# Kernel tuning notes

Measured on AMD Instinct MI355X. Metric: run time of the kernel, lower is better.

The kernel has to match this reference:

```python
import jax, jax.numpy as jnp
import numpy as np

# Scaled-up constants (GRID_SIZE=96)
AFFINE_HIDDEN_DIM = 128
ATTENTION_DIM = 256
EMBEDDING_DIM = 512
MAX_CONTRAST = 1.8
RANGE_SIZE = 4
NUM_RANGE_BLOCKS = 13824   # (96//4)**3
NUM_DOMAIN_BLOCKS = 1728   # (96//8)**3
SOFTMAX_TEMPERATURE = 0.25


def setup_inputs() -> dict:
    key = jax.random.key(0)
    ks = jax.random.split(key, 17)
    E, A, H = EMBEDDING_DIM, ATTENTION_DIM, AFFINE_HIDDEN_DIM
    NR, ND = NUM_RANGE_BLOCKS, NUM_DOMAIN_BLOCKS
    s_lin = 1.0 / np.sqrt(E)  # torch Linear default init scale
    return {
        "pooled_domains": jax.random.normal(ks[0], (ND, RANGE_SIZE, RANGE_SIZE, RANGE_SIZE), jnp.float32),
        "range_latents": jax.random.normal(ks[1], (NR, E), jnp.float32),
        "domain_latents": jax.random.normal(ks[2], (ND, E), jnp.float32),
        "range_positional": jax.random.normal(ks[3], (NR, E), jnp.float32),
        "domain_positional": jax.random.normal(ks[4], (ND, E), jnp.float32),
        "W_rproj": jax.random.normal(ks[5], (E, A), jnp.float32) * s_lin,
        "b_rproj": jax.random.normal(ks[6], (A,), jnp.float32) * s_lin,
        "W_dproj": jax.random.normal(ks[7], (E, A), jnp.float32) * s_lin,
        "b_dproj": jax.random.normal(ks[8], (A,), jnp.float32) * s_lin,
        "W_rcon": jax.random.normal(ks[9], (E, H), jnp.float32) * s_lin,
        "b_rcon": jax.random.normal(ks[10], (H,), jnp.float32) * s_lin,
        "W_dcon": jax.random.normal(ks[11], (E, H), jnp.float32) * s_lin,
        "b_dcon": jax.random.normal(ks[12], (H,), jnp.float32) * s_lin,
        "W_roff": jax.random.normal(ks[13], (E, H), jnp.float32) * s_lin,
        "b_roff": jax.random.normal(ks[14], (H,), jnp.float32) * s_lin,
        "W_doff": jax.random.normal(ks[15], (E, H), jnp.float32) * s_lin,
        "b_doff": jax.random.normal(ks[16], (H,), jnp.float32) * s_lin,
    }


def reference(pooled_domains, range_latents, domain_latents,
              range_positional, domain_positional,
              W_rproj, b_rproj, W_dproj, b_dproj,
              W_rcon, b_rcon, W_dcon, b_dcon,
              W_roff, b_roff, W_doff, b_doff):
    range_base = range_latents + range_positional      # [NR, E]
    domain_base = domain_latents + domain_positional   # [ND, E]

    range_repr = range_base @ W_rproj + b_rproj        # [NR, A]
    domain_repr = domain_base @ W_dproj + b_dproj      # [ND, A]

    inv_sqrt_h = 1.0 / np.sqrt(AFFINE_HIDDEN_DIM).astype(np.float32)
    range_con = range_base @ W_rcon + b_rcon           # [NR, H]
    domain_con = domain_base @ W_dcon + b_dcon         # [ND, H]
    contrast = jnp.tanh((range_con @ domain_con.T) * inv_sqrt_h) * MAX_CONTRAST  # [NR, ND]

    range_off = range_base @ W_roff + b_roff
    domain_off = domain_base @ W_doff + b_doff
    offset = jnp.tanh((range_off @ domain_off.T) * inv_sqrt_h)  # [NR, ND]

    scale = 1.0 / (np.sqrt(ATTENTION_DIM).astype(np.float32) * SOFTMAX_TEMPERATURE)
    logits = (range_repr @ domain_repr.T) * scale      # [NR, ND]
    weights = jax.nn.softmax(logits, axis=-1)          # [NR, ND]

    domain_flat = pooled_domains.reshape(NUM_DOMAIN_BLOCKS, -1)   # [ND, 64]
    scaled_domains = (weights * contrast) @ domain_flat           # [NR, 64]
    offset_effective = jnp.sum(weights * offset, axis=1, keepdims=True)  # [NR, 1]
    decoded = (scaled_domains + offset_effective).reshape(-1, RANGE_SIZE, RANGE_SIZE, RANGE_SIZE)
    return decoded
```

## Files before the change

kernel.cpp:

```cpp
#include <hip/hip_runtime.h>
#include <stdint.h>

#define NRB 13824
#define NDB 1728
#define EDIM 512
#define SPLIT 18
#define DPB (NDB/SPLIT)
#define TILES (DPB/32)

typedef __attribute__((ext_vector_type(8))) _Float16 h8;
typedef __attribute__((ext_vector_type(4))) _Float16 hh4;
typedef __attribute__((ext_vector_type(4))) float f4;
typedef __attribute__((ext_vector_type(4))) unsigned short us4;

typedef __attribute__((address_space(3))) void lds_void;
typedef const __attribute__((address_space(1))) void gbl_void;

#define MFMA(a,b,c) __builtin_amdgcn_mfma_f32_16x16x32_f16(a,b,c,0,0,0)

static __device__ __forceinline__ ushort f2h(float f){
  union { _Float16 h; ushort u; } cv;
  cv.h = (_Float16)f;
  return cv.u;
}

static __device__ __forceinline__ float tanh_fast(float x){
  float ax = __builtin_fabsf(x);
  float t = __builtin_amdgcn_exp2f(ax * -2.8853900817779268f);
  float r = (1.0f - t) * __builtin_amdgcn_rcpf(1.0f + t);
  return __builtin_copysignf(r, x);
}

__global__ void prep_kernel(
    const float* __restrict__ pooled,
    const float* __restrict__ rlat, const float* __restrict__ dlat,
    const float* __restrict__ rpos, const float* __restrict__ dpos,
    const float* __restrict__ Wrp, const float* __restrict__ brp,
    const float* __restrict__ Wdp, const float* __restrict__ bdp,
    const float* __restrict__ Wrc, const float* __restrict__ brc,
    const float* __restrict__ Wdc, const float* __restrict__ bdc,
    const float* __restrict__ Wro, const float* __restrict__ bro,
    const float* __restrict__ Wdo2, const float* __restrict__ bdo2,
    ushort* __restrict__ rb, ushort* __restrict__ db,
    ushort* __restrict__ Wr_t, ushort* __restrict__ Wd_t,
    float* __restrict__ br_c, float* __restrict__ bd_c,
    ushort* __restrict__ dflt)
{
  const int NRE = NRB*EDIM, NDE = NDB*EDIM;
  int i0 = blockIdx.x*blockDim.x + threadIdx.x;
  int stride = gridDim.x*blockDim.x;
  for (int i=i0; i<NRE; i+=stride) rb[i] = f2h(rlat[i]+rpos[i]);
  for (int i=i0; i<NDE; i+=stride) db[i] = f2h(dlat[i]+dpos[i]);
  for (int i=i0; i<512*512; i+=stride){
    int n = i>>9, k = i&511;
    float vr = (n<256) ? Wrp[k*256+n] : ((n<384) ? Wrc[k*128+(n-256)] : Wro[k*128+(n-384)]);
    float vd = (n<256) ? Wdp[k*256+n] : ((n<384) ? Wdc[k*128+(n-256)] : Wdo2[k*128+(n-384)]);
    Wr_t[i] = f2h(vr); Wd_t[i] = f2h(vd);
  }
  for (int i=i0; i<512; i+=stride){
    br_c[i] = (i<256) ? brp[i] : ((i<384) ? brc[i-256] : bro[i-384]);
    bd_c[i] = (i<256) ? bdp[i] : ((i<384) ? bdc[i-256] : bdo2[i-384]);
  }
  for (int i=i0; i<64*NDB; i+=stride){
    int c = i/NDB, d = i - c*NDB;
    dflt[i] = f2h(pooled[d*64+c]);
  }
}

__global__ __launch_bounds__(256) void gemm_feats(
    const ushort* __restrict__ Ar, const ushort* __restrict__ Btr,
    const float* __restrict__ biasr, ushort* __restrict__ Cr,
    const ushort* __restrict__ Ad, const ushort* __restrict__ Btd,
    const float* __restrict__ biasd, ushort* __restrict__ Cd)
{
  const ushort* A;  const ushort* Bt; const float* bias; ushort* C; int M; int bx;
  if ((int)blockIdx.x < 108){ A=Ar; Bt=Btr; bias=biasr; C=Cr; M=NRB; bx=blockIdx.x; }
  else                      { A=Ad; Bt=Btd; bias=biasd; C=Cd; M=NDB; bx=blockIdx.x-108; }

  __shared__ ushort As[128*32];
  __shared__ ushort Bs[128*32];
  const int tid = threadIdx.x;
  const int lane = tid & 63;
  const int wave = tid >> 6;
  const int l15 = lane & 15;
  const int lhi = lane >> 4;
  const int row0 = bx * 128;
  const int col0 = blockIdx.y * 128;
  const int wr = (wave>>1)*64;
  const int wc = (wave&1)*64;

  f4 acc[4][4] = {};
  char* Ab = (char*)As; char* Bb = (char*)Bs;

  for (int k0=0; k0<EDIM; k0+=32){
    __syncthreads();
    #pragma unroll
    for (int c=0;c<2;c++){
      int L = (tid + c*256)*16;
      int r = L>>6;
      int kb = L&63;
      int kbs = kb ^ ((r&3)<<4);
      int ra = row0 + r; if (ra > M-1) ra = M-1;
      const ushort* srcA = A + (size_t)ra*EDIM + k0 + (kbs>>1);
      const ushort* srcB = Bt + (size_t)(col0+r)*EDIM + k0 + (kbs>>1);
      __builtin_amdgcn_global_load_lds((gbl_void*)srcA, (lds_void*)(Ab + L), 16, 0, 0);
      __builtin_amdgcn_global_load_lds((gbl_void*)srcB, (lds_void*)(Bb + L), 16, 0, 0);
    }
    __syncthreads();
    h8 af[4], bf[4];
    #pragma unroll
    for (int i=0;i<4;i++){
      int rowa = wr + i*16 + l15;
      af[i] = *(const h8*)(Ab + (((rowa*64) + lhi*16) ^ ((rowa&3)<<4)));
      int rowb = wc + i*16 + l15;
      bf[i] = *(const h8*)(Bb + (((rowb*64) + lhi*16) ^ ((rowb&3)<<4)));
    }
    #pragma unroll
    for (int i=0;i<4;i++){
      #pragma unroll
      for (int j=0;j<4;j++){
        acc[i][j] = MFMA(af[i], bf[j], acc[i][j]);
      }
    }
  }

  #pragma unroll
  for (int j=0;j<4;j++){
    int col = col0 + wc + j*16 + l15;
    float bv = bias[col];
    #pragma unroll
    for (int i=0;i<4;i++){
      #pragma unroll
      for (int r=0;r<4;r++){
        int row = row0 + wr + i*16 + lhi*4 + r;
        if (row < M) C[(size_t)row*EDIM + col] = f2h(acc[i][j][r] + bv);
      }
    }
  }
}

__global__ __launch_bounds__(512, 2) void attn_kernel(
    const ushort* __restrict__ rfeat,
    const ushort* __restrict__ dfeat,
    const ushort* __restrict__ dflt,
    ushort* __restrict__ accbuf,
    float* __restrict__ mlbuf)
{
  __shared__ ushort DF[DPB*512];
  __shared__ ushort PT[8][16*32];

  const int tid  = threadIdx.x;
  const int wave = tid >> 6;
  const int lane = tid & 63;
  const int l15  = lane & 15;
  const int lhi  = lane >> 4;
  const int wrow = blockIdx.x*128 + wave*16;
  const int by   = blockIdx.y;
  const int dbase = by * DPB;

  constexpr float CL = 0.25f * 1.4426950408889634f;
  constexpr float CH = 0.08838834764831845f;

  char* DFb = (char*)DF;
  char* PTb = (char*)PT[wave];

  #pragma unroll
  for (int c=0;c<12;c++){
    int id = tid + c*512;
    int dom = id >> 6;
    h8 v = *(const h8*)(dfeat + (size_t)(dbase+dom)*EDIM + (id&63)*8);
    *(h8*)(DFb + ((id*16) ^ ((dom&7)<<4))) = v;
  }

  h8 q[16];
  {
    const ushort* qr = rfeat + (size_t)(wrow + l15)*EDIM + lhi*8;
    #pragma unroll
    for (int c=0;c<16;c++) q[c] = *(const h8*)(qr + c*32);
  }

  f4 acc[4] = {};
  float m = -1e30f, lsum = 0.f, offa = 0.f;
  const int sb = (lane & 48) + ((lane >> 4) << 2);

  __syncthreads();

  for (int t=0; t<TILES; ++t){
    const int d0 = dbase + t*32;
    const int dloc = t*32;

    f4 SL[2] = {}, SC[2] = {}, SO[2] = {};
    #pragma unroll
    for (int ct=0; ct<2; ++ct){
      const int dom = dloc + ct*16 + l15;
      const int swz = (dom&7)<<4;
      const int base = dom*1024 + lhi*16;
      #pragma unroll
      for (int c=0;c<8;c++){
        h8 b = *(const h8*)(DFb + ((base + c*64) ^ swz));
        SL[ct] = MFMA(b, q[c], SL[ct]);
      }
      #pragma unroll
      for (int c=8;c<12;c++){
        h8 b = *(const h8*)(DFb + ((base + c*64) ^ swz));
        SC[ct] = MFMA(b, q[c], SC[ct]);
      }
      #pragma unroll
      for (int c=12;c<16;c++){
        h8 b = *(const h8*)(DFb + ((base + c*64) ^ swz));
        SO[ct] = MFMA(b, q[c], SO[ct]);
      }
    }

    float lm = fmaxf(
        fmaxf(fmaxf(SL[0][0],SL[0][1]), fmaxf(SL[0][2],SL[0][3])),
        fmaxf(fmaxf(SL[1][0],SL[1][1]), fmaxf(SL[1][2],SL[1][3]))) * CL;
    lm = fmaxf(lm, __shfl_xor(lm, 16, 64));
    lm = fmaxf(lm, __shfl_xor(lm, 32, 64));
    float mn = fmaxf(m, lm);
    float al = __builtin_amdgcn_exp2f(m - mn);
    m = mn;
    lsum *= al; offa *= al;

    us4 w0, w1;
    #pragma unroll
    for (int r=0;r<4;r++){
      float p0 = __builtin_amdgcn_exp2f(SL[0][r]*CL - mn);
      float p1 = __builtin_amdgcn_exp2f(SL[1][r]*CL - mn);
      lsum += p0 + p1;
      float c0 = tanh_fast(SC[0][r]*CH)*1.8f;
      float c1 = tanh_fast(SC[1][r]*CH)*1.8f;
      float o0 = tanh_fast(SO[0][r]*CH);
      float o1 = tanh_fast(SO[1][r]*CH);
      offa += p0*o0 + p1*o1;
      w0[r] = f2h(p0*c0);
      w1[r] = f2h(p1*c1);
    }
    {
      const int wbase = l15*64;
      const int xs = (l15&3)<<4;
      *(us4*)(PTb + ((wbase + lhi*8) ^ xs))      = w0;
      *(us4*)(PTb + ((wbase + 32 + lhi*8) ^ xs)) = w1;
    }

    __builtin_amdgcn_sched_barrier(0);

    {
      float alr[4];
      #pragma unroll
      for (int r=0;r<4;r++) alr[r] = __shfl(al, sb + r, 64);
      #pragma unroll
      for (int nt=0; nt<4; nt++){
        acc[nt][0]*=alr[0]; acc[nt][1]*=alr[1];
        acc[nt][2]*=alr[2]; acc[nt][3]*=alr[3];
      }
      h8 pa = *(const h8*)(PTb + ((l15*64 + lhi*16) ^ ((l15&3)<<4)));
      #pragma unroll
      for (int nt=0; nt<4; nt++){
        int n = nt*16 + l15;
        h8 vb = *(const h8*)(dflt + (size_t)n*NDB + d0 + lhi*8);
        acc[nt] = MFMA(pa, vb, acc[nt]);
      }
    }

    __builtin_amdgcn_sched_barrier(0);
  }

  float ls = lsum, oa = offa;
  ls += __shfl_xor(ls, 16, 64); ls += __shfl_xor(ls, 32, 64);
  oa += __shfl_xor(oa, 16, 64); oa += __shfl_xor(oa, 32, 64);

  #pragma unroll
  for (int r=0;r<4;r++){
    int row = wrow + lhi*4 + r;
    size_t base = ((size_t)by*NRB + row)*64;
    #pragma unroll
    for (int nt=0; nt<4; nt++){
      accbuf[base + nt*16 + l15] = f2h(acc[nt][r]);
    }
  }
  if (lane < 16){
    size_t mo = ((size_t)by*NRB + wrow + l15)*4;
    mlbuf[mo+0] = m;
    mlbuf[mo+1] = ls;
    mlbuf[mo+2] = oa;
  }
}

#define CROWS 16
__global__ __launch_bounds__(256) void combine_kernel(
    const ushort* __restrict__ accbuf,
    const float* __restrict__ mlbuf,
    float* __restrict__ out)
{
  __shared__ float wS[CROWS][SPLIT+1];
  __shared__ float c0S[CROWS], iTS[CROWS];
  const int rb = blockIdx.x;
  const int tid = threadIdx.x;

  if (tid < CROWS){
    int row = rb*CROWS + tid;
    float M = -1e30f;
    float m[SPLIT], l[SPLIT], o[SPLIT];
    #pragma unroll
    for (int s=0;s<SPLIT;s++){
      size_t off = ((size_t)s*NRB + row)*4;
      m[s]=mlbuf[off]; l[s]=mlbuf[off+1]; o[s]=mlbuf[off+2];
      M = fmaxf(M, m[s]);
    }
    float T=0.f, C=0.f;
    #pragma unroll
    for (int s=0;s<SPLIT;s++){
      float w = __builtin_amdgcn_exp2f(m[s]-M);
      wS[tid][s]=w; T += l[s]*w; C += o[s]*w;
    }
    c0S[tid]=C; iTS[tid]=1.0f/T;
  }
  __syncthreads();

  const int row_l = tid>>4;
  const int cb = (tid&15)*4;
  const int row = rb*CROWS + row_l;
  float res[4] = {};
  #pragma unroll
  for (int s=0;s<SPLIT;s++){
    float w = wS[row_l][s];
    hh4 v = *(const hh4*)(accbuf + ((size_t)s*NRB + row)*64 + cb);
    #pragma unroll
    for (int j=0;j<4;j++) res[j] += (float)v[j]*w;
  }
  float C = c0S[row_l], iT = iTS[row_l];
  #pragma unroll
  for (int j=0;j<4;j++) out[(size_t)row*64 + cb + j] = (res[j]+C)*iT;
}

extern "C" void kernel_launch(void* const* d_in, const int* in_sizes, int n_in,
                              void* d_out, int out_size, void* d_ws, size_t ws_size,
                              hipStream_t stream) {
  const float* pooled = (const float*)d_in[0];
  const float* rlat   = (const float*)d_in[1];
  const float* dlat   = (const float*)d_in[2];
  const float* rpos   = (const float*)d_in[3];
  const float* dpos   = (const float*)d_in[4];
  const float* Wrp    = (const float*)d_in[5];
  const float* brp    = (const float*)d_in[6];
  const float* Wdp    = (const float*)d_in[7];
  const float* bdp    = (const float*)d_in[8];
  const float* Wrc    = (const float*)d_in[9];
  const float* brc    = (const float*)d_in[10];
  const float* Wdc    = (const float*)d_in[11];
  const float* bdc    = (const float*)d_in[12];
  const float* Wro    = (const float*)d_in[13];
  const float* bro    = (const float*)d_in[14];
  const float* Wdo2   = (const float*)d_in[15];
  const float* bdo2   = (const float*)d_in[16];

  char* ws = (char*)d_ws;
  size_t off = 0;
  ushort* rb    = (ushort*)(ws + off); off += (size_t)NRB*EDIM*2;
  ushort* db    = (ushort*)(ws + off); off += (size_t)NDB*EDIM*2;
  ushort* Wr_t  = (ushort*)(ws + off); off += (size_t)512*512*2;
  ushort* Wd_t  = (ushort*)(ws + off); off += (size_t)512*512*2;
  float*  br_c  = (float*)(ws + off);  off += 512*4;
  float*  bd_c  = (float*)(ws + off);  off += 512*4;
  ushort* rfeat = (ushort*)(ws + off); off += (size_t)NRB*EDIM*2;
  ushort* dfeat = (ushort*)(ws + off); off += (size_t)NDB*EDIM*2;
  ushort* dflt  = (ushort*)(ws + off); off += (size_t)64*NDB*2;
  ushort* accb  = (ushort*)(ws + off); off += (size_t)SPLIT*NRB*64*2;
  float*  mlb   = (float*)(ws + off);  off += (size_t)SPLIT*NRB*4*4;

  prep_kernel<<<2048, 256, 0, stream>>>(pooled, rlat, dlat, rpos, dpos,
      Wrp, brp, Wdp, bdp, Wrc, brc, Wdc, bdc, Wro, bro, Wdo2, bdo2,
      rb, db, Wr_t, Wd_t, br_c, bd_c, dflt);

  gemm_feats<<<dim3(122,4), 256, 0, stream>>>(rb, Wr_t, br_c, rfeat,
                                              db, Wd_t, bd_c, dfeat);

  attn_kernel<<<dim3(108, SPLIT), 512, 0, stream>>>(rfeat, dfeat, dflt, accb, mlb);
  combine_kernel<<<NRB/CROWS, 256, 0, stream>>>(accb, mlb, (float*)d_out);
}
```

Measured before the change: 132.9 us.

## Compute all score tiles first and use exact max instead of online softmax

Instead of an online softmax that rescales running sums and the output accumulators after every tile, all score tiles (logits, contrast, offset) are computed up front and kept in registers. A single global row max is taken before the exponentials, which removes the per-tile shuffles, exp of the correction factor and accumulator rescaling. The cost is much higher register pressure, since TILES=3 tiles times three score sets are live at once, which could cut occupancy or cause spills.

```diff
diff --git a/kernel.cpp b/kernel.cpp
--- a/kernel.cpp
+++ b/kernel.cpp
@@ -180,58 +180,65 @@
   }
 
   f4 acc[4] = {};
-  float m = -1e30f, lsum = 0.f, offa = 0.f;
   const int sb = (lane & 48) + ((lane >> 4) << 2);
+  (void)sb;
 
   __syncthreads();
 
+  f4 SL[TILES][2] = {}, SC[TILES][2] = {}, SO[TILES][2] = {};
+  #pragma unroll
+  for (int t=0; t<TILES; ++t){
+    #pragma unroll
+    for (int ct=0; ct<2; ++ct){
+      const int dom = t*32 + ct*16 + l15;
+      const int swz = (dom&7)<<4;
+      const int base = dom*1024 + lhi*16;
+      #pragma unroll
+      for (int c=0;c<8;c++){
+        h8 b = *(const h8*)(DFb + ((base + c*64) ^ swz));
+        SL[t][ct] = MFMA(b, q[c], SL[t][ct]);
+      }
+      #pragma unroll
+      for (int c=8;c<12;c++){
+        h8 b = *(const h8*)(DFb + ((base + c*64) ^ swz));
+        SC[t][ct] = MFMA(b, q[c], SC[t][ct]);
+      }
+      #pragma unroll
+      for (int c=12;c<16;c++){
+        h8 b = *(const h8*)(DFb + ((base + c*64) ^ swz));
+        SO[t][ct] = MFMA(b, q[c], SO[t][ct]);
+      }
+    }
+  }
+
+  float lm = -1e30f;
+  #pragma unroll
+  for (int t=0; t<TILES; ++t){
+    #pragma unroll
+    for (int ct=0; ct<2; ++ct){
+      lm = fmaxf(lm, fmaxf(fmaxf(SL[t][ct][0],SL[t][ct][1]),
+                           fmaxf(SL[t][ct][2],SL[t][ct][3])));
+    }
+  }
+  lm *= CL;
+  lm = fmaxf(lm, __shfl_xor(lm, 16, 64));
+  float m = fmaxf(lm, __shfl_xor(lm, 32, 64));
+  float lsum = 0.f, offa = 0.f;
+
+  #pragma unroll
   for (int t=0; t<TILES; ++t){
     const int d0 = dbase + t*32;
-    const int dloc = t*32;
-
-    f4 SL[2] = {}, SC[2] = {}, SO[2] = {};
-    #pragma unroll
-    for (int ct=0; ct<2; ++ct){
-      const int dom = dloc + ct*16 + l15;
-      const int swz = (dom&7)<<4;
-      const int base = dom*1024 + lhi*16;
-      #pragma unroll
-      for (int c=0;c<8;c++){
-        h8 b = *(const h8*)(DFb + ((base + c*64) ^ swz));
-        SL[ct] = MFMA(b, q[c], SL[ct]);
-      }
-      #pragma unroll
-      for (int c=8;c<12;c++){
-        h8 b = *(const h8*)(DFb + ((base + c*64) ^ swz));
-        SC[ct] = MFMA(b, q[c], SC[ct]);
-      }
-      #pragma unroll
-      for (int c=12;c<16;c++){
-        h8 b = *(const h8*)(DFb + ((base + c*64) ^ swz));
-        SO[ct] = MFMA(b, q[c], SO[ct]);
-      }
-    }
-
-    float lm = fmaxf(
-        fmaxf(fmaxf(SL[0][0],SL[0][1]), fmaxf(SL[0][2],SL[0][3])),
-        fmaxf(fmaxf(SL[1][0],SL[1][1]), fmaxf(SL[1][2],SL[1][3]))) * CL;
-    lm = fmaxf(lm, __shfl_xor(lm, 16, 64));
-    lm = fmaxf(lm, __shfl_xor(lm, 32, 64));
-    float mn = fmaxf(m, lm);
-    float al = __builtin_amdgcn_exp2f(m - mn);
-    m = mn;
-    lsum *= al; offa *= al;
 
     us4 w0, w1;
     #pragma unroll
     for (int r=0;r<4;r++){
-      float p0 = __builtin_amdgcn_exp2f(SL[0][r]*CL - mn);
-      float p1 = __builtin_amdgcn_exp2f(SL[1][r]*CL - mn);
+      float p0 = __builtin_amdgcn_exp2f(SL[t][0][r]*CL - m);
+      float p1 = __builtin_amdgcn_exp2f(SL[t][1][r]*CL - m);
       lsum += p0 + p1;
-      float c0 = tanh_fast(SC[0][r]*CH)*1.8f;
-      float c1 = tanh_fast(SC[1][r]*CH)*1.8f;
-      float o0 = tanh_fast(SO[0][r]*CH);
-      float o1 = tanh_fast(SO[1][r]*CH);
+      float c0 = tanh_fast(SC[t][0][r]*CH)*1.8f;
+      float c1 = tanh_fast(SC[t][1][r]*CH)*1.8f;
+      float o0 = tanh_fast(SO[t][0][r]*CH);
+      float o1 = tanh_fast(SO[t][1][r]*CH);
       offa += p0*o0 + p1*o1;
       w0[r] = f2h(p0*c0);
       w1[r] = f2h(p1*c1);
@@ -246,14 +253,6 @@
     __builtin_amdgcn_sched_barrier(0);
 
     {
-      float alr[4];
-      #pragma unroll
-      for (int r=0;r<4;r++) alr[r] = __shfl(al, sb + r, 64);
-      #pragma unroll
-      for (int nt=0; nt<4; nt++){
-        acc[nt][0]*=alr[0]; acc[nt][1]*=alr[1];
-        acc[nt][2]*=alr[2]; acc[nt][3]*=alr[3];
-      }
       h8 pa = *(const h8*)(PTb + ((l15*64 + lhi*16) ^ ((l15&3)<<4)));
       #pragma unroll
       for (int nt=0; nt<4; nt++){
```

After: 137.3 us. +3.3%, slower.
